# Kernel optimization log

Measured on AMD Instinct MI355X. Metric: run time of the kernel, lower is better.

Reference implementation:

```python
import jax, jax.numpy as jnp
import numpy as np

N = 294912          # total points, divisible by patch size
C = 128             # channels
H = 8               # num_heads
K = 48              # patch_size
D = C // H          # head dim = 16
POS_BND = int((4 * K) ** (1.0 / 3.0) * 2)   # = 11
RPE_NUM = 2 * POS_BND + 1                    # = 23
SCALE = D ** -0.5


def setup_inputs() -> dict:
    key = jax.random.key(0)
    ks = jax.random.split(key, 8)
    feat = jax.random.normal(ks[0], (N, C), dtype=jnp.float32)
    # serialized order is a permutation of the points; inverse undoes it
    order = jax.random.permutation(ks[1], N).astype(jnp.int32)
    inverse = jnp.argsort(order).astype(jnp.int32)
    grid_coord = jax.random.randint(ks[2], (N, 3), 0, 1024, dtype=jnp.int32)
    w_qkv = jax.random.normal(ks[3], (3 * C, C), dtype=jnp.float32) * 0.02
    b_qkv = jnp.zeros((3 * C,), jnp.float32)
    w_proj = jax.random.normal(ks[4], (C, C), dtype=jnp.float32) * 0.02
    b_proj = jnp.zeros((C,), jnp.float32)
    rpe_table = jax.random.normal(ks[5], (3 * RPE_NUM, H), dtype=jnp.float32) * 0.02
    return {
        "feat": feat, "w_qkv": w_qkv, "b_qkv": b_qkv,
        "w_proj": w_proj, "b_proj": b_proj, "rpe_table": rpe_table,
        "order": order, "inverse": inverse, "grid_coord": grid_coord,
    }


def reference(feat, w_qkv, b_qkv, w_proj, b_proj, rpe_table, order, inverse, grid_coord):
    P = N // K  # number of serialized patches
    # qkv projection then irregular gather by serialized order
    qkv = (feat @ w_qkv.T + b_qkv)[order]                 # [N, 3C]
    qkv = qkv.reshape(P, K, 3, H, D)
    q = qkv[:, :, 0]                                      # [P, K, H, D]
    k = qkv[:, :, 1]
    v = qkv[:, :, 2]
    # upcast attention: scores in float32
    attn = jnp.einsum(
        "pkhd,pmhd->phkm",
        q.astype(jnp.float32) * SCALE,
        k.astype(jnp.float32),
    )                                                     # [P, H, K, K]
    # RPE bias: per-patch relative voxel offsets -> table lookup
    gc = grid_coord[order].reshape(P, K, 3)
    rel = gc[:, :, None, :] - gc[:, None, :, :]           # [P, K, K, 3]
    idx = jnp.clip(rel, -POS_BND, POS_BND) + POS_BND + jnp.arange(3) * RPE_NUM
    bias = rpe_table[idx].sum(axis=3)                     # [P, K, K, H]
    attn = attn + bias.transpose(0, 3, 1, 2)              # [P, H, K, K]
    attn = jax.nn.softmax(attn, axis=-1).astype(qkv.dtype)
    out = jnp.einsum("phkm,pmhd->pkhd", attn, v)          # [P, K, H, D]
    out = out.reshape(N, C)
    # scatter back via inverse indices, then output projection
    out = out[inverse] @ w_proj.T + b_proj
    return out
```

## Files before the change

### kernel.cpp

```cpp
#include <hip/hip_runtime.h>

#define NPTS 294912
#define CDIM 128
#define HH 8
#define KPATCH 48
#define DD 16
#define NP (NPTS / KPATCH)
#define POS_BND 11
#define RPE_NUM 23
#define RPE_ROWS (3 * RPE_NUM)
#define QSCALE 0.25f

typedef __attribute__((ext_vector_type(8))) short short8v;
typedef __attribute__((ext_vector_type(4))) short short4v;
typedef __attribute__((ext_vector_type(4))) float f32x4;
typedef __attribute__((ext_vector_type(4))) float f4v;

__device__ __align__(16) unsigned short g_whi[65536];
__device__ __align__(16) unsigned short g_wlo[65536];

#define UNI_BYTES 36864
#define KOFF 12288
#define VOFF 24576

__device__ __forceinline__ unsigned short bf16r(float x) {
    unsigned u = __float_as_uint(x);
    return (unsigned short)((u + 0x7fffu + ((u >> 16) & 1u)) >> 16);
}

__device__ __forceinline__ void split8(const float* x, short8v& hi, short8v& lo) {
    #pragma unroll
    for (int i = 0; i < 8; ++i) {
        unsigned u = __float_as_uint(x[i]);
        hi[i] = (short)(u >> 16);
        float l = x[i] - __uint_as_float(u & 0xffff0000u);
        lo[i] = (short)(__float_as_uint(l) >> 16);
    }
}

__global__ __launch_bounds__(256) void prep_w(const float* __restrict__ w_qkv,
                                              const float* __restrict__ w_proj) {
    int gid = blockIdx.x * 256 + threadIdx.x;
    float x[4];
    if (gid < 12288) *(f4v*)x = ((const f4v*)w_qkv)[gid];
    else             *(f4v*)x = ((const f4v*)w_proj)[gid - 12288];
    short4v hi, lo;
    #pragma unroll
    for (int i = 0; i < 4; ++i) {
        unsigned short h = bf16r(x[i]);
        hi[i] = (short)h;
        float hf = __uint_as_float((unsigned)h << 16);
        lo[i] = (short)bf16r(x[i] - hf);
    }
    *(short4v*)&g_whi[gid * 4] = hi;
    *(short4v*)&g_wlo[gid * 4] = lo;
}

__global__ __launch_bounds__(512, 4) void fused_patch_attn(
    const float* __restrict__ feat,
    const float* __restrict__ b_qkv,
    const float* __restrict__ b_proj,
    const float* __restrict__ rpe,
    const int* __restrict__ order,
    const int* __restrict__ grid_coord,
    float* __restrict__ out)
{
    __shared__ int ord[KPATCH];
    __shared__ int gcl[KPATCH][3];
    __shared__ float rpe_t[HH * RPE_ROWS];
    __shared__ __align__(16) char uni[UNI_BYTES];

    const int p    = blockIdx.x;
    const int tid  = threadIdx.x;
    const int wid  = tid >> 6;
    const int lane = tid & 63;
    const int lrow = lane & 15;
    const int lgrp = lane >> 4;

    if (tid < KPATCH) {
        int o = order[p * KPATCH + tid];
        ord[tid] = o;
        gcl[tid][0] = grid_coord[o * 3 + 0];
        gcl[tid][1] = grid_coord[o * 3 + 1];
        gcl[tid][2] = grid_coord[o * 3 + 2];
    }
    for (int e = tid; e < HH * RPE_ROWS; e += 512) {
        int h = e / RPE_ROWS;
        int i = e - h * RPE_ROWS;
        rpe_t[e] = rpe[i * HH + h];
    }
    __syncthreads();

    for (int e = tid; e < KPATCH * 16; e += 512) {
        int r  = e >> 4;
        int c8 = e & 15;
        const float* src = feat + (size_t)ord[r] * CDIM + c8 * 8;
        float x[8];
        *(f4v*)(x)     = __builtin_nontemporal_load((const f4v*)src);
        *(f4v*)(x + 4) = __builtin_nontemporal_load((const f4v*)(src + 4));
        short8v hi, lo;
        split8(x, hi, lo);
        int addr = (r * 256 + c8 * 16) ^ ((r & 7) << 4);
        *(short8v*)(uni + addr)        = hi;
        *(short8v*)(uni + KOFF + addr) = lo;
    }
    __syncthreads();

    f32x4 acc[3][3];
    #pragma unroll
    for (int i = 0; i < 3; ++i)
        #pragma unroll
        for (int j = 0; j < 3; ++j) acc[i][j] = (f32x4)0.0f;

    #pragma unroll
    for (int ks = 0; ks < 4; ++ks) {
        short8v aH[3], aL[3];
        #pragma unroll
        for (int mt = 0; mt < 3; ++mt) {
            int row  = mt * 16 + lrow;
            int boff = (row * 256 + ks * 64 + lgrp * 16) ^ ((row & 7) << 4);
            aH[mt] = *(const short8v*)(uni + boff);
            aL[mt] = *(const short8v*)(uni + KOFF + boff);
        }
        #pragma unroll
        for (int nt = 0; nt < 3; ++nt) {
            int NT = wid * 3 + nt;
            short8v bH = *(const short8v*)&g_whi[(NT * 16 + lrow) * CDIM + ks * 32 + lgrp * 8];
            #pragma unroll
            for (int mt = 0; mt < 3; ++mt) {
                acc[mt][nt] = __builtin_amdgcn_mfma_f32_16x16x32_bf16(aH[mt], bH, acc[mt][nt], 0, 0, 0);
                acc[mt][nt] = __builtin_amdgcn_mfma_f32_16x16x32_bf16(aL[mt], bH, acc[mt][nt], 0, 0, 0);
            }
        }
    }
    __syncthreads();

    #pragma unroll
    for (int nt = 0; nt < 3; ++nt) {
        int NT   = wid * 3 + nt;
        int type = NT >> 3;
        int hh   = NT & 7;
        int d    = lrow;
        float bq = b_qkv[NT * 16 + lrow];
        float scale = (type == 0) ? QSCALE : 1.0f;
        #pragma unroll
        for (int mt = 0; mt < 3; ++mt)
            #pragma unroll
            for (int r = 0; r < 4; ++r) {
                int m = mt * 16 + lgrp * 4 + r;
                unsigned short b = bf16r((acc[mt][nt][r] + bq) * scale);
                int addr;
                if (type < 2) {
                    addr = type * KOFF + hh * 1536 + m * 32
                         + (((d >> 2) ^ (m >> 2)) & 3) * 8 + (d & 3) * 2;
                } else {
                    int mb = m >> 2;
                    addr = VOFF + hh * 1536 + d * 96
                         + (((mb & ~3) | ((mb ^ (d >> 2)) & 3))) * 8 + (m & 3) * 2;
                }
                *(unsigned short*)(uni + addr) = b;
            }
    }
    __syncthreads();

    const int h = wid;
    const float* rbase = &rpe_t[h * RPE_ROWS];
    f32x4 oall[3];
    {
        short8v kf[3], qf[3];
        #pragma unroll
        for (int t = 0; t < 3; ++t) {
            int row = t * 16 + lrow;
            int ra  = row * 32 + (((lgrp ^ (row >> 2)) & 3)) * 8;
            short4v kq = *(const short4v*)(uni + KOFF + h * 1536 + ra);
            short4v qq = *(const short4v*)(uni +        h * 1536 + ra);
            short8v a, b;
            a[0]=kq[0]; a[1]=kq[1]; a[2]=kq[2]; a[3]=kq[3]; a[4]=0; a[5]=0; a[6]=0; a[7]=0;
            b[0]=qq[0]; b[1]=qq[1]; b[2]=qq[2]; b[3]=qq[3]; b[4]=0; b[5]=0; b[6]=0; b[7]=0;
            kf[t] = a; qf[t] = b;
        }
        f32x4 s[3][3];
        #pragma unroll
        for (int qt = 0; qt < 3; ++qt)
            #pragma unroll
            for (int mt = 0; mt < 3; ++mt)
                s[qt][mt] = __builtin_amdgcn_mfma_f32_16x16x32_bf16(kf[mt], qf[qt], (f32x4)0.0f, 0, 0, 0);

        #pragma unroll
        for (int qt = 0; qt < 3; ++qt) {
            int q  = qt * 16 + lrow;
            int gx = gcl[q][0], gy = gcl[q][1], gz = gcl[q][2];
            #pragma unroll
            for (int mt = 0; mt < 3; ++mt)
                #pragma unroll
                for (int r = 0; r < 4; ++r) {
                    int m  = mt * 16 + lgrp * 4 + r;
                    int rx = gx - gcl[m][0];
                    int ry = gy - gcl[m][1];
                    int rz = gz - gcl[m][2];
                    rx = rx < -POS_BND ? -POS_BND : (rx > POS_BND ? POS_BND : rx);
                    ry = ry < -POS_BND ? -POS_BND : (ry > POS_BND ? POS_BND : ry);
                    rz = rz < -POS_BND ? -POS_BND : (rz > POS_BND ? POS_BND : rz);
                    s[qt][mt][r] += rbase[rx + POS_BND]
                                  + rbase[ry + POS_BND + RPE_NUM]
                                  + rbase[rz + POS_BND + 2 * RPE_NUM];
                }
        }

        #pragma unroll
        for (int qt = 0; qt < 3; ++qt) {
            float mx = -1e30f;
            #pragma unroll
            for (int mt = 0; mt < 3; ++mt)
                #pragma unroll
                for (int r = 0; r < 4; ++r) mx = fmaxf(mx, s[qt][mt][r]);
            mx = fmaxf(mx, __shfl_xor(mx, 16));
            mx = fmaxf(mx, __shfl_xor(mx, 32));
            float sum = 0.f;
            #pragma unroll
            for (int mt = 0; mt < 3; ++mt)
                #pragma unroll
                for (int r = 0; r < 4; ++r) {
                    float e = __expf(s[qt][mt][r] - mx);
                    s[qt][mt][r] = e;
                    sum += e;
                }
            sum += __shfl_xor(sum, 16);
            sum += __shfl_xor(sum, 32);
            float inv = 1.0f / sum;
            #pragma unroll
            for (int mt = 0; mt < 3; ++mt)
                #pragma unroll
                for (int r = 0; r < 4; ++r) s[qt][mt][r] *= inv;
        }

        short8v vb0, vb1;
        {
            int base = VOFF + h * 1536 + lrow * 96 + (((lgrp ^ (lrow >> 2)) & 3)) * 8;
            short4v x0 = *(const short4v*)(uni + base);
            short4v x1 = *(const short4v*)(uni + base + 32);
            short4v x2 = *(const short4v*)(uni + base + 64);
            vb0[0]=x0[0]; vb0[1]=x0[1]; vb0[2]=x0[2]; vb0[3]=x0[3];
            vb0[4]=x1[0]; vb0[5]=x1[1]; vb0[6]=x1[2]; vb0[7]=x1[3];
            vb1[0]=x2[0]; vb1[1]=x2[1]; vb1[2]=x2[2]; vb1[3]=x2[3];
            vb1[4]=0; vb1[5]=0; vb1[6]=0; vb1[7]=0;
        }
        #pragma unroll
        for (int qt = 0; qt < 3; ++qt) {
            short8v pa0, pa1;
            #pragma unroll
            for (int j = 0; j < 4; ++j) {
                pa0[j]     = (short)bf16r(s[qt][0][j]);
                pa0[4 + j] = (short)bf16r(s[qt][1][j]);
                pa1[j]     = (short)bf16r(s[qt][2][j]);
                pa1[4 + j] = 0;
            }
            f32x4 o = __builtin_amdgcn_mfma_f32_16x16x32_bf16(pa0, vb0, (f32x4)0.0f, 0, 0, 0);
            o = __builtin_amdgcn_mfma_f32_16x16x32_bf16(pa1, vb1, o, 0, 0, 0);
            oall[qt] = o;
        }
    }
    __syncthreads();

    {
        int c = wid * 16 + lrow;
        #pragma unroll
        for (int qt = 0; qt < 3; ++qt)
            #pragma unroll
            for (int r = 0; r < 4; ++r) {
                int q = qt * 16 + lgrp * 4 + r;
                float x = oall[qt][r];
                unsigned u = __float_as_uint(x);
                unsigned short h16 = (unsigned short)(u >> 16);
                float lres = x - __uint_as_float(u & 0xffff0000u);
                unsigned short l16 = (unsigned short)(__float_as_uint(lres) >> 16);
                int addr = (q * 256 + c * 2) ^ ((q & 7) << 4);
                *(unsigned short*)(uni + addr)        = h16;
                *(unsigned short*)(uni + KOFF + addr) = l16;
            }
    }
    __syncthreads();

    f32x4 pacc[3];
    #pragma unroll
    for (int i = 0; i < 3; ++i) pacc[i] = (f32x4)0.0f;

    #pragma unroll
    for (int ks = 0; ks < 4; ++ks) {
        short8v aH[3], aL[3];
        #pragma unroll
        for (int mt = 0; mt < 3; ++mt) {
            int row  = mt * 16 + lrow;
            int boff = (row * 256 + ks * 64 + lgrp * 16) ^ ((row & 7) << 4);
            aH[mt] = *(const short8v*)(uni + boff);
            aL[mt] = *(const short8v*)(uni + KOFF + boff);
        }
        int woff = 49152 + (wid * 16 + lrow) * CDIM + ks * 32 + lgrp * 8;
        short8v bH = *(const short8v*)&g_whi[woff];
        short8v bL = *(const short8v*)&g_wlo[woff];
        #pragma unroll
        for (int mt = 0; mt < 3; ++mt) {
            pacc[mt] = __builtin_amdgcn_mfma_f32_16x16x32_bf16(aH[mt], bH, pacc[mt], 0, 0, 0);
            pacc[mt] = __builtin_amdgcn_mfma_f32_16x16x32_bf16(aL[mt], bH, pacc[mt], 0, 0, 0);
            pacc[mt] = __builtin_amdgcn_mfma_f32_16x16x32_bf16(aH[mt], bL, pacc[mt], 0, 0, 0);
        }
    }

    {
        int c  = wid * 16 + lrow;
        float bp = b_proj[c];
        #pragma unroll
        for (int mt = 0; mt < 3; ++mt)
            #pragma unroll
            for (int r = 0; r < 4; ++r) {
                int row = mt * 16 + lgrp * 4 + r;
                out[(size_t)ord[row] * CDIM + c] = pacc[mt][r] + bp;
            }
    }
}

extern "C" void kernel_launch(void* const* d_in, const int* in_sizes, int n_in,
                              void* d_out, int out_size, void* d_ws, size_t ws_size,
                              hipStream_t stream) {
    const float* feat   = (const float*)d_in[0];
    const float* w_qkv  = (const float*)d_in[1];
    const float* b_qkv  = (const float*)d_in[2];
    const float* w_proj = (const float*)d_in[3];
    const float* b_proj = (const float*)d_in[4];
    const float* rpe    = (const float*)d_in[5];
    const int*   order  = (const int*)d_in[6];
    const int*   gc     = (const int*)d_in[8];
    float* out = (float*)d_out;

    prep_w<<<64, 256, 0, stream>>>(w_qkv, w_proj);
    fused_patch_attn<<<NP, 512, 0, stream>>>(feat, b_qkv, b_proj, rpe, order, gc, out);
}
```

Measured before the change: 217.6 us.

## Precompute packed RPE indices per patch and vectorize V-tile stores

```diff
diff --git a/kernel.cpp b/kernel.cpp
--- a/kernel.cpp
+++ b/kernel.cpp
@@ -10,6 +10,7 @@
 #define RPE_NUM 23
 #define RPE_ROWS (3 * RPE_NUM)
 #define QSCALE 0.25f
+#define IDXS 49
 
 typedef __attribute__((ext_vector_type(8))) short short8v;
 typedef __attribute__((ext_vector_type(4))) short short4v;
@@ -36,6 +37,10 @@
         float l = x[i] - __uint_as_float(u & 0xffff0000u);
         lo[i] = (short)(__float_as_uint(l) >> 16);
     }
+}
+
+__device__ __forceinline__ int clampi(int x) {
+    return min(max(x, -POS_BND), POS_BND);
 }
 
 __global__ __launch_bounds__(256) void prep_w(const float* __restrict__ w_qkv,
@@ -56,7 +61,7 @@
     *(short4v*)&g_wlo[gid * 4] = lo;
 }
 
-__global__ __launch_bounds__(512, 4) void fused_patch_attn(
+__global__ __launch_bounds__(512, 6) void fused_patch_attn(
     const float* __restrict__ feat,
     const float* __restrict__ b_qkv,
     const float* __restrict__ b_proj,
@@ -68,6 +73,7 @@
     __shared__ int ord[KPATCH];
     __shared__ int gcl[KPATCH][3];
     __shared__ float rpe_t[HH * RPE_ROWS];
+    __shared__ unsigned idx_l[KPATCH * IDXS];
     __shared__ __align__(16) char uni[UNI_BYTES];
 
     const int p    = blockIdx.x;
@@ -104,6 +110,14 @@
         *(short8v*)(uni + addr)        = hi;
         *(short8v*)(uni + KOFF + addr) = lo;
     }
+    for (int e = tid; e < KPATCH * KPATCH; e += 512) {
+        int q = e / KPATCH;
+        int m = e - q * KPATCH;
+        int b0 = clampi(gcl[q][0] - gcl[m][0]) + POS_BND;
+        int b1 = clampi(gcl[q][1] - gcl[m][1]) + POS_BND + RPE_NUM;
+        int b2 = clampi(gcl[q][2] - gcl[m][2]) + POS_BND + 2 * RPE_NUM;
+        idx_l[q * IDXS + m] = (unsigned)(b0 | (b1 << 8) | (b2 << 16));
+    }
     __syncthreads();
 
     f32x4 acc[3][3];
@@ -144,22 +158,27 @@
         float bq = b_qkv[NT * 16 + lrow];
         float scale = (type == 0) ? QSCALE : 1.0f;
         #pragma unroll
-        for (int mt = 0; mt < 3; ++mt)
-            #pragma unroll
-            for (int r = 0; r < 4; ++r) {
-                int m = mt * 16 + lgrp * 4 + r;
-                unsigned short b = bf16r((acc[mt][nt][r] + bq) * scale);
-                int addr;
-                if (type < 2) {
-                    addr = type * KOFF + hh * 1536 + m * 32
-                         + (((d >> 2) ^ (m >> 2)) & 3) * 8 + (d & 3) * 2;
-                } else {
-                    int mb = m >> 2;
-                    addr = VOFF + hh * 1536 + d * 96
-                         + (((mb & ~3) | ((mb ^ (d >> 2)) & 3))) * 8 + (m & 3) * 2;
-                }
-                *(unsigned short*)(uni + addr) = b;
-            }
+        for (int mt = 0; mt < 3; ++mt) {
+            unsigned short s0 = bf16r((acc[mt][nt][0] + bq) * scale);
+            unsigned short s1 = bf16r((acc[mt][nt][1] + bq) * scale);
+            unsigned short s2 = bf16r((acc[mt][nt][2] + bq) * scale);
+            unsigned short s3 = bf16r((acc[mt][nt][3] + bq) * scale);
+            int m0 = mt * 16 + lgrp * 4;
+            if (type < 2) {
+                int base = type * KOFF + hh * 1536 + (d & 3) * 2;
+                int sw0  = (((d >> 2) ^ (m0 >> 2)) & 3) * 8;
+                *(unsigned short*)(uni + base + (m0 + 0) * 32 + sw0) = s0;
+                *(unsigned short*)(uni + base + (m0 + 1) * 32 + sw0) = s1;
+                *(unsigned short*)(uni + base + (m0 + 2) * 32 + sw0) = s2;
+                *(unsigned short*)(uni + base + (m0 + 3) * 32 + sw0) = s3;
+            } else {
+                int mb = m0 >> 2;
+                int addr = VOFF + hh * 1536 + d * 96
+                         + (((mb & ~3) | ((mb ^ (d >> 2)) & 3))) * 8;
+                *(unsigned*)(uni + addr)     = (unsigned)s0 | ((unsigned)s1 << 16);
+                *(unsigned*)(uni + addr + 4) = (unsigned)s2 | ((unsigned)s3 << 16);
+            }
+        }
     }
     __syncthreads();
 
@@ -188,22 +207,15 @@
 
         #pragma unroll
         for (int qt = 0; qt < 3; ++qt) {
-            int q  = qt * 16 + lrow;
-            int gx = gcl[q][0], gy = gcl[q][1], gz = gcl[q][2];
+            const unsigned* iq = &idx_l[(qt * 16 + lrow) * IDXS];
             #pragma unroll
             for (int mt = 0; mt < 3; ++mt)
                 #pragma unroll
                 for (int r = 0; r < 4; ++r) {
-                    int m  = mt * 16 + lgrp * 4 + r;
-                    int rx = gx - gcl[m][0];
-                    int ry = gy - gcl[m][1];
-                    int rz = gz - gcl[m][2];
-                    rx = rx < -POS_BND ? -POS_BND : (rx > POS_BND ? POS_BND : rx);
-                    ry = ry < -POS_BND ? -POS_BND : (ry > POS_BND ? POS_BND : ry);
-                    rz = rz < -POS_BND ? -POS_BND : (rz > POS_BND ? POS_BND : rz);
-                    s[qt][mt][r] += rbase[rx + POS_BND]
-                                  + rbase[ry + POS_BND + RPE_NUM]
-                                  + rbase[rz + POS_BND + 2 * RPE_NUM];
+                    unsigned v = iq[mt * 16 + lgrp * 4 + r];
+                    s[qt][mt][r] += rbase[v & 255]
+                                  + rbase[(v >> 8) & 255]
+                                  + rbase[v >> 16];
                 }
         }
 
```

After: 246.6 us. 1.13x slower.
